# Kernel tuning notes

Hardware: AMD Instinct MI355X
Metric: run time of the kernel (lower is better)

## Reference

```python
import jax, jax.numpy as jnp
import numpy as np

BS, GRID, D, WS, NH = 4, 64, 1024, 8, 16
N = GRID * GRID            # num_patch
DH = D // NH               # head dim
SHIFT = WS // 2
NWIN = (GRID // WS) ** 2   # num_window
LW = WS * WS               # num_patch_in_window


def _layer_norm(x, g, b, eps=1e-5):
    mu = jnp.mean(x, -1, keepdims=True)
    var = jnp.var(x, -1, keepdims=True)
    return (x - mu) * jax.lax.rsqrt(var + eps) * g + b


def _window_partition(x, bs):
    # [bs, N, D] -> [bs*NWIN, LW, D]
    x = x.reshape(bs, GRID // WS, WS, GRID // WS, WS, D)
    x = x.transpose(0, 1, 3, 2, 4, 5)
    return x.reshape(bs * NWIN, LW, D)


def _window_merge(w, bs):
    # [bs*NWIN, LW, D] -> [bs, N, D]
    w = w.reshape(bs, GRID // WS, GRID // WS, WS, WS, D)
    w = w.transpose(0, 1, 3, 2, 4, 5)
    return w.reshape(bs, N, D)


def _mhsa(x, wqkv, bqkv, wo, bo, mask=None):
    # x: [B, L, D]; standard multi-head self-attention
    B, L, _ = x.shape
    qkv = x @ wqkv + bqkv                              # [B, L, 3D]
    q, k, v = jnp.split(qkv, 3, axis=-1)
    q = q.reshape(B, L, NH, DH).transpose(0, 2, 1, 3)  # [B, H, L, dh]
    k = k.reshape(B, L, NH, DH).transpose(0, 2, 1, 3)
    v = v.reshape(B, L, NH, DH).transpose(0, 2, 1, 3)
    scores = jnp.einsum('bhld,bhmd->bhlm', q, k) / jnp.sqrt(jnp.float32(DH))
    if mask is not None:
        scores = scores + mask                         # additive -1e9 mask
    prob = jax.nn.softmax(scores, axis=-1)
    out = jnp.einsum('bhlm,bhmd->bhld', prob, v)
    out = out.transpose(0, 2, 1, 3).reshape(B, L, D)
    return out @ wo + bo


def _shift_mask():
    # canonical Swin shifted-window attention mask (static, numpy at trace time)
    img = np.zeros((GRID, GRID), np.int32)
    cnt = 0
    sls = (slice(0, -WS), slice(-WS, -SHIFT), slice(-SHIFT, None))
    for hs in sls:
        for ws_ in sls:
            img[hs, ws_] = cnt
            cnt += 1
    win = img.reshape(GRID // WS, WS, GRID // WS, WS).transpose(0, 2, 1, 3).reshape(NWIN, LW)
    m = np.where(win[:, :, None] != win[:, None, :], -1e9, 0.0).astype(np.float32)
    return jnp.asarray(m)  # [NWIN, LW, LW]


def setup_inputs() -> dict:
    key = jax.random.key(0)
    ks = iter(jax.random.split(key, 40))
    def w(shape, scale=0.02):
        return jax.random.normal(next(ks), shape, jnp.float32) * scale
    inp = {"x": jax.random.normal(next(ks), (BS, N, D), jnp.float32)}
    for nm in ["ln1", "ln2", "ln3", "ln4"]:
        inp[nm + "_g"] = jnp.ones((D,), jnp.float32)
        inp[nm + "_b"] = jnp.zeros((D,), jnp.float32)
    for nm in ["mlp1a", "mlp2a"]:
        inp[nm + "_w"] = w((D, 4 * D)); inp[nm + "_b"] = jnp.zeros((4 * D,), jnp.float32)
    for nm in ["mlp1b", "mlp2b"]:
        inp[nm + "_w"] = w((4 * D, D)); inp[nm + "_b"] = jnp.zeros((D,), jnp.float32)
    for nm in ["a1", "a2"]:
        inp[nm + "_wqkv"] = w((D, 3 * D)); inp[nm + "_bqkv"] = jnp.zeros((3 * D,), jnp.float32)
        inp[nm + "_wo"] = w((D, D)); inp[nm + "_bo"] = jnp.zeros((D,), jnp.float32)
    return inp


def reference(x, ln1_g, ln1_b, ln2_g, ln2_b, ln3_g, ln3_b, ln4_g, ln4_b,
              mlp1a_w, mlp1a_b, mlp1b_w, mlp1b_b, mlp2a_w, mlp2a_b, mlp2b_w, mlp2b_b,
              a1_wqkv, a1_bqkv, a1_wo, a1_bo, a2_wqkv, a2_bqkv, a2_wo, a2_bo):
    bs = x.shape[0]
    # --- layer 1: W-MSA + MLP (no activation between the two Linears, per source) ---
    inp1 = _layer_norm(x, ln1_g, ln1_b)
    w = _window_partition(inp1, bs)
    w = _mhsa(w, a1_wqkv, a1_bqkv, a1_wo, a1_bo)
    w = inp1 + _window_merge(w, bs)
    out1 = _layer_norm(w, ln2_g, ln2_b) @ mlp1a_w + mlp1a_b
    out1 = out1 @ mlp1b_w + mlp1b_b + w
    # --- layer 2: SW-MSA + MLP ---
    inp2 = _layer_norm(out1, ln3_g, ln3_b)
    img = inp2.reshape(bs, GRID, GRID, D)
    img = jnp.roll(img, (-SHIFT, -SHIFT), axis=(1, 2)).reshape(bs, N, D)
    sw = _window_partition(img, bs)
    mask = jnp.tile(_shift_mask(), (bs, 1, 1))[:, None]  # [bs*NWIN, 1, LW, LW]
    sw = _mhsa(sw, a2_wqkv, a2_bqkv, a2_wo, a2_bo, mask=mask)
    sw = _window_merge(sw, bs).reshape(bs, GRID, GRID, D)
    sw = jnp.roll(sw, (SHIFT, SHIFT), axis=(1, 2)).reshape(bs, N, D)
    sw = out1 + sw
    out2 = _layer_norm(sw, ln4_g, ln4_b) @ mlp2a_w + mlp2a_b
    out2 = out2 @ mlp2b_w + mlp2b_b + sw
    return out2.reshape(bs, NWIN, LW, D)
```

## Files before the change

### kernel.cpp

```cpp
#include <hip/hip_runtime.h>


typedef __bf16 bf16x8 __attribute__((ext_vector_type(8)));
typedef float f32x4 __attribute__((ext_vector_type(4)));

__device__ __forceinline__ unsigned short f2b(float x) {
  union { float f; unsigned u; } c; c.f = x;
  unsigned r = c.u + 0x7fffu + ((c.u >> 16) & 1u);
  return (unsigned short)(r >> 16);
}

__device__ __forceinline__ void gload16(const void* gp, void* lp) {
  __builtin_amdgcn_global_load_lds(
      (const __attribute__((address_space(1))) void*)gp,
      (__attribute__((address_space(3))) void*)lp, 16, 0, 0);
}

__global__ void wconv(const float* __restrict__ src, unsigned short* __restrict__ dst,
                      int K, int N) {
  __shared__ float t[32][33];
  const int tx = threadIdx.x, ty = threadIdx.y;
  const int n0 = blockIdx.x * 32, k0 = blockIdx.y * 32;
#pragma unroll
  for (int i = 0; i < 4; ++i)
    t[ty + i * 8][tx] = src[(size_t)(k0 + ty + i * 8) * N + n0 + tx];
  __syncthreads();
#pragma unroll
  for (int i = 0; i < 4; ++i)
    dst[(size_t)(n0 + ty + i * 8) * K + k0 + tx] = f2b(t[tx][ty + i * 8]);
}

__global__ __launch_bounds__(256) void ln_fused(
    const float* __restrict__ in, const float* __restrict__ gw,
    const float* __restrict__ bw, float* __restrict__ outf,
    unsigned short* __restrict__ outb) {
  const int row = blockIdx.x;
  const int t = threadIdx.x;
  const int w = t >> 6, l = t & 63;
  const float4 v = ((const float4*)(in + (size_t)row * 1024))[t];
  float s1 = v.x + v.y + v.z + v.w;
  float s2 = v.x * v.x + v.y * v.y + v.z * v.z + v.w * v.w;
#pragma unroll
  for (int d = 32; d >= 1; d >>= 1) { s1 += __shfl_down(s1, d); s2 += __shfl_down(s2, d); }
  __shared__ float red[8];
  if (l == 0) { red[w] = s1; red[4 + w] = s2; }
  __syncthreads();
  const float S1 = red[0] + red[1] + red[2] + red[3];
  const float S2 = red[4] + red[5] + red[6] + red[7];
  const float mu = S1 * (1.0f / 1024.0f);
  const float rsg = rsqrtf(S2 * (1.0f / 1024.0f) - mu * mu + 1e-5f);
  const float4 g4 = ((const float4*)gw)[t];
  const float4 b4 = ((const float4*)bw)[t];
  float4 y;
  y.x = (v.x - mu) * rsg * g4.x + b4.x;
  y.y = (v.y - mu) * rsg * g4.y + b4.y;
  y.z = (v.z - mu) * rsg * g4.z + b4.z;
  y.w = (v.w - mu) * rsg * g4.w + b4.w;
  if (outf) ((float4*)(outf + (size_t)row * 1024))[t] = y;
  ushort4 ob;
  ob.x = f2b(y.x); ob.y = f2b(y.y); ob.z = f2b(y.z); ob.w = f2b(y.w);
  ((ushort4*)(outb + (size_t)row * 1024))[t] = ob;
}

template <int EPI>
__global__ __launch_bounds__(256, 3) void gemm_bt(
    const unsigned short* __restrict__ A, const unsigned short* __restrict__ BT,
    const float* __restrict__ bias, const float* __restrict__ res,
    void* __restrict__ Cout, int M, int N, int K) {
  __shared__ __align__(16) char lds[16384];
  char* ldsA = lds;
  char* ldsB = lds + 8192;
  const int tid = threadIdx.x;
  const int w = tid >> 6, l = tid & 63;
  const int lhi = l >> 4, llo = l & 15;
  const int cpx = gridDim.x >> 3;
  const int bid = (blockIdx.x & 7) * cpx + (blockIdx.x >> 3);
  const int tiles_n = N >> 7;
  const int tm = bid / tiles_n;
  const int tn = bid - tm * tiles_n;
  const int wr = w >> 1, wc = w & 1;

  size_t aoff[2], boff[2];
  int ldst[2];
#pragma unroll
  for (int p = 0; p < 2; ++p) {
    const int g = tid + p * 256;
    const int row = g >> 2;
    const int sl = (g & 3) ^ ((row >> 1) & 3);
    aoff[p] = (size_t)(tm * 128 + row) * K + sl * 8;
    boff[p] = (size_t)(tn * 128 + row) * K + sl * 8;
    ldst[p] = p * 4096 + w * 1024;
  }

  f32x4 acc[4][4] = {};
  for (int k0 = 0; k0 < K; k0 += 32) {
    gload16(A + aoff[0] + k0, ldsA + ldst[0]);
    gload16(A + aoff[1] + k0, ldsA + ldst[1]);
    gload16(BT + boff[0] + k0, ldsB + ldst[0]);
    gload16(BT + boff[1] + k0, ldsB + ldst[1]);
    __syncthreads();
    bf16x8 af[4], bg[4];
#pragma unroll
    for (int m = 0; m < 4; ++m) {
      const int row = wr * 64 + m * 16 + llo;
      const int sl = lhi ^ ((row >> 1) & 3);
      af[m] = *(const bf16x8*)(ldsA + row * 64 + sl * 16);
    }
#pragma unroll
    for (int n = 0; n < 4; ++n) {
      const int row = wc * 64 + n * 16 + llo;
      const int sl = lhi ^ ((row >> 1) & 3);
      bg[n] = *(const bf16x8*)(ldsB + row * 64 + sl * 16);
    }
#pragma unroll
    for (int m = 0; m < 4; ++m)
#pragma unroll
      for (int n = 0; n < 4; ++n)
        acc[m][n] = __builtin_amdgcn_mfma_f32_16x16x32_bf16(af[m], bg[n], acc[m][n], 0, 0, 0);
    __syncthreads();
  }

  const int row0 = tm * 128 + wr * 64 + lhi * 4;
  const int col0 = tn * 128 + wc * 64 + llo;
#pragma unroll
  for (int m = 0; m < 4; ++m)
#pragma unroll
    for (int j = 0; j < 4; ++j) {
      const int rowg = row0 + m * 16 + j;
#pragma unroll
      for (int n = 0; n < 4; ++n) {
        const int colg = col0 + n * 16;
        float v = acc[m][n][j] + bias[colg];
        if (EPI == 1) {
          v += res[(size_t)rowg * N + colg];
          ((float*)Cout)[(size_t)rowg * N + colg] = v;
        } else {
          ((unsigned short*)Cout)[(size_t)rowg * N + colg] = f2b(v);
        }
      }
    }
}

template <int MASKED>
__global__ __launch_bounds__(256, 2) void attn_win(
    const unsigned short* __restrict__ qkv, unsigned short* __restrict__ out) {
  __shared__ __align__(16) char lds[65536];
  const int tid = threadIdx.x;
  const int w = tid >> 6, l = tid & 63;
  const int lhi = l >> 4, llo = l & 15;
  const int head = ((blockIdx.x & 3) << 2) | w;
  const int widx = blockIdx.x >> 2;
  const int batch = widx >> 6;
  const int wy = (widx >> 3) & 7, wx = widx & 7;
  char* Qb = lds + w * 16384;
  char* Kb = Qb + 8192;
  const int lr = l >> 3, lc = l & 7;

  uint4 vv[8];
#pragma unroll
  for (int it = 0; it < 8; ++it) {
    const int r = it * 8 + lr;
    int y = wy * 8 + (r >> 3), x = wx * 8 + (r & 7);
    if (MASKED) { y = (y + 4) & 63; x = (x + 4) & 63; }
    const size_t base = ((size_t)batch * 4096 + y * 64 + x) * 3072 + head * 64 + lc * 8;
    const uint4 qv = *(const uint4*)(qkv + base);
    const uint4 kv = *(const uint4*)(qkv + base + 1024);
    vv[it] = *(const uint4*)(qkv + base + 2048);
    const int sl = lc ^ (r & 7);
    *(uint4*)(Qb + r * 128 + sl * 16) = qv;
    *(uint4*)(Kb + r * 128 + sl * 16) = kv;
  }

  f32x4 s[4][4] = {};
#pragma unroll
  for (int ks = 0; ks < 2; ++ks) {
    bf16x8 aq[4], bk[4];
#pragma unroll
    for (int m = 0; m < 4; ++m) {
      const int r = m * 16 + llo;
      const int sl = (ks * 4 + lhi) ^ (r & 7);
      aq[m] = *(const bf16x8*)(Qb + r * 128 + sl * 16);
    }
#pragma unroll
    for (int n = 0; n < 4; ++n) {
      const int r = n * 16 + llo;
      const int sl = (ks * 4 + lhi) ^ (r & 7);
      bk[n] = *(const bf16x8*)(Kb + r * 128 + sl * 16);
    }
#pragma unroll
    for (int m = 0; m < 4; ++m)
#pragma unroll
      for (int n = 0; n < 4; ++n)
        s[m][n] = __builtin_amdgcn_mfma_f32_16x16x32_bf16(aq[m], bk[n], s[m][n], 0, 0, 0);
  }

  int kg[4] = {0, 0, 0, 0};
  if (MASKED) {
#pragma unroll
    for (int n = 0; n < 4; ++n) {
      const int p = n * 16 + llo;
      const int y = wy * 8 + (p >> 3), x = wx * 8 + (p & 7);
      kg[n] = ((y < 56) ? 0 : ((y < 60) ? 1 : 2)) * 3 + ((x < 56) ? 0 : ((x < 60) ? 1 : 2));
    }
  }
  float rs[4][4];
#pragma unroll
  for (int m = 0; m < 4; ++m)
#pragma unroll
    for (int j = 0; j < 4; ++j) {
      const int qi = m * 16 + lhi * 4 + j;
      int qg = 0;
      if (MASKED) {
        const int y = wy * 8 + (qi >> 3), x = wx * 8 + (qi & 7);
        qg = ((y < 56) ? 0 : ((y < 60) ? 1 : 2)) * 3 + ((x < 56) ? 0 : ((x < 60) ? 1 : 2));
      }
      float mx = -3e38f;
#pragma unroll
      for (int n = 0; n < 4; ++n) {
        float v = s[m][n][j] * 0.125f;
        if (MASKED && kg[n] != qg) v -= 1e9f;
        s[m][n][j] = v;
        mx = fmaxf(mx, v);
      }
#pragma unroll
      for (int d = 1; d < 16; d <<= 1) mx = fmaxf(mx, __shfl_xor(mx, d));
      float sm = 0.f;
#pragma unroll
      for (int n = 0; n < 4; ++n) {
        const float e = __expf(s[m][n][j] - mx);
        s[m][n][j] = e;
        sm += e;
      }
#pragma unroll
      for (int d = 1; d < 16; d <<= 1) sm += __shfl_xor(sm, d);
      rs[m][j] = sm;
    }

#pragma unroll
  for (int m = 0; m < 4; ++m)
#pragma unroll
    for (int j = 0; j < 4; ++j) {
      const int qi = m * 16 + lhi * 4 + j;
#pragma unroll
      for (int n = 0; n < 4; ++n) {
        const int kc = n * 16 + llo;
        *(unsigned short*)(Kb + qi * 128 + (((kc >> 3) ^ (qi & 7)) << 4) + (kc & 7) * 2) =
            f2b(s[m][n][j]);
      }
    }
#pragma unroll
  for (int it = 0; it < 8; ++it) {
    const int r = it * 8 + lr;
    const unsigned short* pv = (const unsigned short*)&vv[it];
#pragma unroll
    for (int e = 0; e < 8; ++e) {
      const int d = lc * 8 + e;
      *(unsigned short*)(Qb + d * 128 + (((r >> 3) ^ (d & 7)) << 4) + (r & 7) * 2) = pv[e];
    }
  }

  f32x4 o[4][4] = {};
#pragma unroll
  for (int ks = 0; ks < 2; ++ks) {
    bf16x8 ap[4], bv[4];
#pragma unroll
    for (int m = 0; m < 4; ++m) {
      const int r = m * 16 + llo;
      const int sl = (ks * 4 + lhi) ^ (r & 7);
      ap[m] = *(const bf16x8*)(Kb + r * 128 + sl * 16);
    }
#pragma unroll
    for (int n = 0; n < 4; ++n) {
      const int r = n * 16 + llo;
      const int sl = (ks * 4 + lhi) ^ (r & 7);
      bv[n] = *(const bf16x8*)(Qb + r * 128 + sl * 16);
    }
#pragma unroll
    for (int m = 0; m < 4; ++m)
#pragma unroll
      for (int n = 0; n < 4; ++n)
        o[m][n] = __builtin_amdgcn_mfma_f32_16x16x32_bf16(ap[m], bv[n], o[m][n], 0, 0, 0);
  }

#pragma unroll
  for (int m = 0; m < 4; ++m)
#pragma unroll
    for (int j = 0; j < 4; ++j) {
      const int qi = m * 16 + lhi * 4 + j;
      int y = wy * 8 + (qi >> 3), x = wx * 8 + (qi & 7);
      if (MASKED) { y = (y + 4) & 63; x = (x + 4) & 63; }
      const size_t prow = (size_t)batch * 4096 + y * 64 + x;
      const float inv = 1.0f / rs[m][j];
#pragma unroll
      for (int n = 0; n < 4; ++n)
        out[prow * 1024 + head * 64 + n * 16 + llo] = f2b(o[m][n][j] * inv);
    }
}

extern "C" void kernel_launch(void* const* d_in, const int* in_sizes, int n_in,
                              void* d_out, int out_size, void* d_ws, size_t ws_size,
                              hipStream_t stream) {
  (void)in_sizes; (void)n_in; (void)out_size;
  const float* x       = (const float*)d_in[0];
  const float* ln1g    = (const float*)d_in[1];
  const float* ln1b    = (const float*)d_in[2];
  const float* ln2g    = (const float*)d_in[3];
  const float* ln2b    = (const float*)d_in[4];
  const float* ln3g    = (const float*)d_in[5];
  const float* ln3b    = (const float*)d_in[6];
  const float* ln4g    = (const float*)d_in[7];
  const float* ln4b    = (const float*)d_in[8];
  const float* mlp1a_w = (const float*)d_in[9];
  const float* mlp1a_b = (const float*)d_in[10];
  const float* mlp2a_w = (const float*)d_in[11];
  const float* mlp2a_b = (const float*)d_in[12];
  const float* mlp1b_w = (const float*)d_in[13];
  const float* mlp1b_b = (const float*)d_in[14];
  const float* mlp2b_w = (const float*)d_in[15];
  const float* mlp2b_b = (const float*)d_in[16];
  const float* a1_wqkv = (const float*)d_in[17];
  const float* a1_bqkv = (const float*)d_in[18];
  const float* a1_wo   = (const float*)d_in[19];
  const float* a1_bo   = (const float*)d_in[20];
  const float* a2_wqkv = (const float*)d_in[21];
  const float* a2_bqkv = (const float*)d_in[22];
  const float* a2_wo   = (const float*)d_in[23];
  const float* a2_bo   = (const float*)d_in[24];

  const size_t MB = 1048576;
  char* ws = (char*)d_ws;
  unsigned short* wqkv1T = (unsigned short*)(ws);
  unsigned short* wo1T   = (unsigned short*)(ws + 6291456);
  unsigned short* wm1aT  = (unsigned short*)(ws + 8388608);
  unsigned short* wm1bT  = (unsigned short*)(ws + 16777216);
  unsigned short* wqkv2T = (unsigned short*)(ws + 25165824);
  unsigned short* wo2T   = (unsigned short*)(ws + 31457280);
  unsigned short* wm2aT  = (unsigned short*)(ws + 33554432);
  unsigned short* wm2bT  = (unsigned short*)(ws + 41943040);
  float*          F2     = (float*)(ws + 48 * MB);
  unsigned short* X      = (unsigned short*)(ws + 112 * MB);
  char*           S      = ws + 144 * MB;
  float*          F1     = (float*)d_out;

  const size_t avail = ws_size > 144 * MB ? ws_size - 144 * MB : 0;
  const int NB = (avail >= 128 * MB) ? 4 : (avail >= 64 * MB) ? 2 : 1;
  const int MC = NB * 4096;
  unsigned short* Sq = (unsigned short*)S;
  unsigned short* Sa = (unsigned short*)(S + (size_t)MC * 3072 * 2);
  unsigned short* Sm = (unsigned short*)S;

  const dim3 tb(32, 8);
  wconv<<<dim3(96, 32), tb, 0, stream>>>(a1_wqkv, wqkv1T, 1024, 3072);
  wconv<<<dim3(32, 32), tb, 0, stream>>>(a1_wo, wo1T, 1024, 1024);
  wconv<<<dim3(128, 32), tb, 0, stream>>>(mlp1a_w, wm1aT, 1024, 4096);
  wconv<<<dim3(32, 128), tb, 0, stream>>>(mlp1b_w, wm1bT, 4096, 1024);
  wconv<<<dim3(96, 32), tb, 0, stream>>>(a2_wqkv, wqkv2T, 1024, 3072);
  wconv<<<dim3(32, 32), tb, 0, stream>>>(a2_wo, wo2T, 1024, 1024);
  wconv<<<dim3(128, 32), tb, 0, stream>>>(mlp2a_w, wm2aT, 1024, 4096);
  wconv<<<dim3(32, 128), tb, 0, stream>>>(mlp2b_w, wm2bT, 4096, 1024);

  ln_fused<<<16384, 256, 0, stream>>>(x, ln1g, ln1b, F1, X);
  for (int b = 0; b < 4; b += NB) {
    const size_t r0 = (size_t)b * 4096;
    gemm_bt<0><<<(MC / 128) * 24, 256, 0, stream>>>(X + r0 * 1024, wqkv1T,
        a1_bqkv, nullptr, Sq, MC, 3072, 1024);
    attn_win<0><<<NB * 256, 256, 0, stream>>>(Sq, Sa);
    gemm_bt<1><<<(MC / 128) * 8, 256, 0, stream>>>(Sa, wo1T, a1_bo,
        F1 + r0 * 1024, F2 + r0 * 1024, MC, 1024, 1024);
  }
  ln_fused<<<16384, 256, 0, stream>>>(F2, ln2g, ln2b, nullptr, X);
  for (int c = 0; c < 4; c += NB) {
    const size_t r0 = (size_t)c * 4096;
    gemm_bt<0><<<(MC / 128) * 32, 256, 0, stream>>>(X + r0 * 1024, wm1aT,
        mlp1a_b, nullptr, Sm, MC, 4096, 1024);
    gemm_bt<1><<<(MC / 128) * 8, 256, 0, stream>>>(Sm, wm1bT, mlp1b_b,
        F2 + r0 * 1024, F1 + r0 * 1024, MC, 1024, 4096);
  }

  ln_fused<<<16384, 256, 0, stream>>>(F1, ln3g, ln3b, nullptr, X);
  for (int b = 0; b < 4; b += NB) {
    const size_t r0 = (size_t)b * 4096;
    gemm_bt<0><<<(MC / 128) * 24, 256, 0, stream>>>(X + r0 * 1024, wqkv2T,
        a2_bqkv, nullptr, Sq, MC, 3072, 1024);
    attn_win<1><<<NB * 256, 256, 0, stream>>>(Sq, Sa);
    gemm_bt<1><<<(MC / 128) * 8, 256, 0, stream>>>(Sa, wo2T, a2_bo,
        F1 + r0 * 1024, F2 + r0 * 1024, MC, 1024, 1024);
  }
  ln_fused<<<16384, 256, 0, stream>>>(F2, ln4g, ln4b, nullptr, X);
  for (int c = 0; c < 4; c += NB) {
    const size_t r0 = (size_t)c * 4096;
    gemm_bt<0><<<(MC / 128) * 32, 256, 0, stream>>>(X + r0 * 1024, wm2aT,
        mlp2a_b, nullptr, Sm, MC, 4096, 1024);
    gemm_bt<1><<<(MC / 128) * 8, 256, 0, stream>>>(Sm, wm2bT, mlp2b_b,
        F2 + r0 * 1024, F1 + r0 * 1024, MC, 1024, 4096);
  }
}
```

Before: 1.446 ms.

## Replace GEMM with 5-stage LDS ring-buffered 128x256 tile kernel

```diff
diff --git a/kernel.cpp b/kernel.cpp
--- a/kernel.cpp
+++ b/kernel.cpp
@@ -62,66 +62,95 @@
   ((ushort4*)(outb + (size_t)row * 1024))[t] = ob;
 }
 
+#define VMWAIT(N) asm volatile("s_waitcnt vmcnt(" #N ")" ::: "memory")
+
+#define GSTEP(VMC, STG, KS)                                                    \
+  {                                                                            \
+    VMWAIT(VMC);                                                               \
+    __builtin_amdgcn_s_barrier();                                              \
+    if (STG) {                                                                 \
+      const size_t ko = (size_t)(KS) * 32;                                     \
+      gload16(A + a_src + ko, lds + ro_s + lds_lane);                          \
+      gload16(BT + b_src0 + ko, lds + ro_s + 8192 + lds_lane);                 \
+      gload16(BT + b_src1 + ko, lds + ro_s + 16384 + lds_lane);                \
+      ro_s += 24576; if (ro_s == 122880) ro_s = 0;                             \
+    }                                                                          \
+    bf16x8 af[4], bf[4];                                                       \
+    _Pragma("unroll")                                                          \
+    for (int m = 0; m < 4; ++m) af[m] = *(const bf16x8*)(lds + ro_r + a_rd[m]);\
+    _Pragma("unroll")                                                          \
+    for (int n = 0; n < 4; ++n) bf[n] = *(const bf16x8*)(lds + ro_r + b_rd[n]);\
+    __builtin_amdgcn_s_setprio(1);                                             \
+    _Pragma("unroll")                                                          \
+    for (int m = 0; m < 4; ++m)                                                \
+      _Pragma("unroll")                                                        \
+      for (int n = 0; n < 4; ++n)                                              \
+        acc[m][n] = __builtin_amdgcn_mfma_f32_16x16x32_bf16(af[m], bf[n],      \
+                                                            acc[m][n], 0, 0, 0);\
+    __builtin_amdgcn_s_setprio(0);                                             \
+    ro_r += 24576; if (ro_r == 122880) ro_r = 0;                               \
+  }
+
 template <int EPI>
-__global__ __launch_bounds__(256, 3) void gemm_bt(
+__global__ __launch_bounds__(512, 2) void gemm_ring(
     const unsigned short* __restrict__ A, const unsigned short* __restrict__ BT,
     const float* __restrict__ bias, const float* __restrict__ res,
     void* __restrict__ Cout, int M, int N, int K) {
-  __shared__ __align__(16) char lds[16384];
-  char* ldsA = lds;
-  char* ldsB = lds + 8192;
+  __shared__ __align__(16) char lds[122880];
   const int tid = threadIdx.x;
   const int w = tid >> 6, l = tid & 63;
   const int lhi = l >> 4, llo = l & 15;
   const int cpx = gridDim.x >> 3;
   const int bid = (blockIdx.x & 7) * cpx + (blockIdx.x >> 3);
-  const int tiles_n = N >> 7;
+  const int tiles_n = N >> 8;
   const int tm = bid / tiles_n;
   const int tn = bid - tm * tiles_n;
-  const int wr = w >> 1, wc = w & 1;
-
-  size_t aoff[2], boff[2];
-  int ldst[2];
-#pragma unroll
-  for (int p = 0; p < 2; ++p) {
-    const int g = tid + p * 256;
-    const int row = g >> 2;
-    const int sl = (g & 3) ^ ((row >> 1) & 3);
-    aoff[p] = (size_t)(tm * 128 + row) * K + sl * 8;
-    boff[p] = (size_t)(tn * 128 + row) * K + sl * 8;
-    ldst[p] = p * 4096 + w * 1024;
-  }
+  const int wr = w >> 2, wc = w & 3;
+
+  const int ga_row = tid >> 2;
+  const int ga_g = (tid & 3) ^ ((ga_row >> 1) & 3);
+  const size_t a_src = (size_t)(tm * 128 + ga_row) * K + ga_g * 8;
+  const int gb0_row = tid >> 2;
+  const int gb0_g = (tid & 3) ^ ((gb0_row >> 1) & 3);
+  const size_t b_src0 = (size_t)(tn * 256 + gb0_row) * K + gb0_g * 8;
+  const int gb1_row = (512 + tid) >> 2;
+  const int gb1_g = (tid & 3) ^ ((gb1_row >> 1) & 3);
+  const size_t b_src1 = (size_t)(tn * 256 + gb1_row) * K + gb1_g * 8;
+  const int lds_lane = w * 1024;
+
+  int a_rd[4], b_rd[4];
+#pragma unroll
+  for (int m = 0; m < 4; ++m) {
+    const int row = wr * 64 + m * 16 + llo;
+    a_rd[m] = row * 64 + ((lhi ^ ((row >> 1) & 3)) << 4);
+  }
+#pragma unroll
+  for (int n = 0; n < 4; ++n) {
+    const int row = wc * 64 + n * 16 + llo;
+    b_rd[n] = 8192 + row * 64 + ((lhi ^ ((row >> 1) & 3)) << 4);
+  }
+
+  int ro_s = 0;
+#pragma unroll
+  for (int p = 0; p < 4; ++p) {
+    const size_t ko = (size_t)p * 32;
+    gload16(A + a_src + ko, lds + ro_s + lds_lane);
+    gload16(BT + b_src0 + ko, lds + ro_s + 8192 + lds_lane);
+    gload16(BT + b_src1 + ko, lds + ro_s + 16384 + lds_lane);
+    ro_s += 24576;
+  }
+  int ro_r = 0;
 
   f32x4 acc[4][4] = {};
-  for (int k0 = 0; k0 < K; k0 += 32) {
-    gload16(A + aoff[0] + k0, ldsA + ldst[0]);
-    gload16(A + aoff[1] + k0, ldsA + ldst[1]);
-    gload16(BT + boff[0] + k0, ldsB + ldst[0]);
-    gload16(BT + boff[1] + k0, ldsB + ldst[1]);
-    __syncthreads();
-    bf16x8 af[4], bg[4];
-#pragma unroll
-    for (int m = 0; m < 4; ++m) {
-      const int row = wr * 64 + m * 16 + llo;
-      const int sl = lhi ^ ((row >> 1) & 3);
-      af[m] = *(const bf16x8*)(ldsA + row * 64 + sl * 16);
-    }
-#pragma unroll
-    for (int n = 0; n < 4; ++n) {
-      const int row = wc * 64 + n * 16 + llo;
-      const int sl = lhi ^ ((row >> 1) & 3);
-      bg[n] = *(const bf16x8*)(ldsB + row * 64 + sl * 16);
-    }
-#pragma unroll
-    for (int m = 0; m < 4; ++m)
-#pragma unroll
-      for (int n = 0; n < 4; ++n)
-        acc[m][n] = __builtin_amdgcn_mfma_f32_16x16x32_bf16(af[m], bg[n], acc[m][n], 0, 0, 0);
-    __syncthreads();
-  }
+  const int ns = K >> 5;
+  for (int s = 0; s < ns - 4; ++s) GSTEP(9, 1, s + 4);
+  GSTEP(9, 0, 0);
+  GSTEP(6, 0, 0);
+  GSTEP(3, 0, 0);
+  GSTEP(0, 0, 0);
 
   const int row0 = tm * 128 + wr * 64 + lhi * 4;
-  const int col0 = tn * 128 + wc * 64 + llo;
+  const int col0 = tn * 256 + wc * 64 + llo;
 #pragma unroll
   for (int m = 0; m < 4; ++m)
 #pragma unroll
@@ -345,6 +374,7 @@
   const size_t avail = ws_size > 144 * MB ? ws_size - 144 * MB : 0;
   const int NB = (avail >= 128 * MB) ? 4 : (avail >= 64 * MB) ? 2 : 1;
   const int MC = NB * 4096;
+  const int MT = MC / 128;
   unsigned short* Sq = (unsigned short*)S;
   unsigned short* Sa = (unsigned short*)(S + (size_t)MC * 3072 * 2);
   unsigned short* Sm = (unsigned short*)S;
@@ -362,36 +392,36 @@
   ln_fused<<<16384, 256, 0, stream>>>(x, ln1g, ln1b, F1, X);
   for (int b = 0; b < 4; b += NB) {
     const size_t r0 = (size_t)b * 4096;
-    gemm_bt<0><<<(MC / 128) * 24, 256, 0, stream>>>(X + r0 * 1024, wqkv1T,
+    gemm_ring<0><<<MT * 12, 512, 0, stream>>>(X + r0 * 1024, wqkv1T,
         a1_bqkv, nullptr, Sq, MC, 3072, 1024);
     attn_win<0><<<NB * 256, 256, 0, stream>>>(Sq, Sa);
-    gemm_bt<1><<<(MC / 128) * 8, 256, 0, stream>>>(Sa, wo1T, a1_bo,
+    gemm_ring<1><<<MT * 4, 512, 0, stream>>>(Sa, wo1T, a1_bo,
         F1 + r0 * 1024, F2 + r0 * 1024, MC, 1024, 1024);
   }
   ln_fused<<<16384, 256, 0, stream>>>(F2, ln2g, ln2b, nullptr, X);
   for (int c = 0; c < 4; c += NB) {
     const size_t r0 = (size_t)c * 4096;
-    gemm_bt<0><<<(MC / 128) * 32, 256, 0, stream>>>(X + r0 * 1024, wm1aT,
+    gemm_ring<0><<<MT * 16, 512, 0, stream>>>(X + r0 * 1024, wm1aT,
         mlp1a_b, nullptr, Sm, MC, 4096, 1024);
-    gemm_bt<1><<<(MC / 128) * 8, 256, 0, stream>>>(Sm, wm1bT, mlp1b_b,
+    gemm_ring<1><<<MT * 4, 512, 0, stream>>>(Sm, wm1bT, mlp1b_b,
         F2 + r0 * 1024, F1 + r0 * 1024, MC, 1024, 4096);
   }
 
   ln_fused<<<16384, 256, 0, stream>>>(F1, ln3g, ln3b, nullptr, X);
   for (int b = 0; b < 4; b += NB) {
     const size_t r0 = (size_t)b * 4096;
-    gemm_bt<0><<<(MC / 128) * 24, 256, 0, stream>>>(X + r0 * 1024, wqkv2T,
+    gemm_ring<0><<<MT * 12, 512, 0, stream>>>(X + r0 * 1024, wqkv2T,
         a2_bqkv, nullptr, Sq, MC, 3072, 1024);
     attn_win<1><<<NB * 256, 256, 0, stream>>>(Sq, Sa);
-    gemm_bt<1><<<(MC / 128) * 8, 256, 0, stream>>>(Sa, wo2T, a2_bo,
+    gemm_ring<1><<<MT * 4, 512, 0, stream>>>(Sa, wo2T, a2_bo,
         F1 + r0 * 1024, F2 + r0 * 1024, MC, 1024, 1024);
   }
   ln_fused<<<16384, 256, 0, stream>>>(F2, ln4g, ln4b, nullptr, X);
   for (int c = 0; c < 4; c += NB) {
     const size_t r0 = (size_t)c * 4096;
-    gemm_bt<0><<<(MC / 128) * 32, 256, 0, stream>>>(X + r0 * 1024, wm2aT,
+    gemm_ring<0><<<MT * 16, 512, 0, stream>>>(X + r0 * 1024, wm2aT,
         mlp2a_b, nullptr, Sm, MC, 4096, 1024);
-    gemm_bt<1><<<(MC / 128) * 8, 256, 0, stream>>>(Sm, wm2bT, mlp2b_b,
+    gemm_ring<1><<<MT * 4, 512, 0, stream>>>(Sm, wm2bT, mlp2b_b,
         F2 + r0 * 1024, F1 + r0 * 1024, MC, 1024, 4096);
   }
 }
```

New measurement: 1.404 ms. -2.9%, faster.
